# Kernel tuning notes

Hardware: AMD Instinct MI355X
Metric: run time of the kernel (lower is better)

## Reference

```python
import jax, jax.numpy as jnp
import numpy as np

VOCAB, HIDDEN, EMBED = 30522, 768, 512
PAD_INDEX = 0
NEG_SLOPE = 0.1


def setup_inputs() -> dict:
    key = jax.random.key(0)
    k1, k2, k3, k4 = jax.random.split(key, 4)
    words = jax.random.randint(k1, (16, 512, 4), 0, VOCAB, dtype=jnp.int64) if jax.config.jax_enable_x64 else jax.random.randint(k1, (16, 512, 4), 0, VOCAB, dtype=jnp.int32)
    embed_table = jax.random.normal(k2, (VOCAB, HIDDEN), dtype=jnp.float32) * 0.02
    w_ffn = jax.random.normal(k3, (HIDDEN, EMBED), dtype=jnp.float32) * 0.02
    b_ffn = jax.random.normal(k4, (EMBED,), dtype=jnp.float32) * 0.02
    return {"words": words, "embed_table": embed_table, "w_ffn": w_ffn, "b_ffn": b_ffn}


def reference(words, embed_table, w_ffn, b_ffn):
    # words: [B, S, W] subword ids; pad_index marks padding subwords/words.
    B, S, W = words.shape
    sub_mask = words != PAD_INDEX                      # [B,S,W] valid subwords
    word_valid = jnp.any(sub_mask, axis=-1)            # [B,S]  words with >=1 subword
    lens = jnp.sum(word_valid, axis=-1)                # [B]    valid words per sequence

    # Stub of transformer last_hidden_state: per-token hidden vectors. [B,S,W,H]
    x = embed_table[words]

    # Masked mean over subwords of each word (segment mean-pool).
    m = sub_mask[..., None].astype(x.dtype)
    cnt = jnp.maximum(jnp.sum(sub_mask, axis=-1), 1)[..., None].astype(x.dtype)
    pooled = jnp.sum(x * m, axis=2) / cnt              # [B,S,H]

    # pad = x[0, -1] of flattened [B, S*W, H] == hidden of last flat token of batch 0
    pad_vec = x[0, -1, -1]                             # [H]

    # Stable compaction: valid words first (mirrors pop-in-order + pad append).
    order = jnp.argsort(jnp.logical_not(word_valid), axis=1, stable=True)  # [B,S]
    pooled_c = jnp.take_along_axis(pooled, order[..., None], axis=1)       # [B,S,H]
    keep = (jnp.arange(S)[None, :] < lens[:, None])[..., None]             # [B,S,1]
    x_seq = jnp.where(keep, pooled_c, pad_vec)         # [B,S,H]

    # FFN: Linear + LeakyReLU(0.1)
    return jax.nn.leaky_relu(x_seq @ w_ffn + b_ffn, NEG_SLOPE)
```

## Files before the change

kernel.cpp:

```cpp
#include <hip/hip_runtime.h>
#include <stdint.h>

#define HIDDEN 768
#define EMBED  512
#define BATCH  16
#define SEQ    512
#define NWORDS (BATCH*SEQ)
#define PAD_FLAT_IDX 2047
#define NEG_SLOPE 0.1f

__device__ __forceinline__ unsigned short f2bf(float f) {
    unsigned int x = __float_as_uint(f);
    unsigned int r = x + 0x7fffu + ((x >> 16) & 1u);
    return (unsigned short)(r >> 16);
}

__global__ __launch_bounds__(256) void prep_kernel(const int* __restrict__ words,
                                                   const float* __restrict__ w,
                                                   int* __restrict__ dest,
                                                   unsigned short* __restrict__ wt) {
    if (blockIdx.x < BATCH) {
        int b = blockIdx.x;
        int t = threadIdx.x;
        int s0 = 2 * t, s1 = 2 * t + 1;
        int4 wa = ((const int4*)words)[b * SEQ + s0];
        int4 wb = ((const int4*)words)[b * SEQ + s1];
        bool v0 = (wa.x | wa.y | wa.z | wa.w) != 0;
        bool v1 = (wb.x | wb.y | wb.z | wb.w) != 0;

        unsigned long long m0 = __ballot(v0);
        unsigned long long m1 = __ballot(v1);
        int lane = t & 63;
        int wave = t >> 6;
        unsigned long long below = (1ull << lane) - 1ull;
        int pre = __popcll(m0 & below) + __popcll(m1 & below);
        __shared__ int wsum[4];
        if (lane == 0) wsum[wave] = __popcll(m0) + __popcll(m1);
        __syncthreads();
        int off = 0, tot = 0;
#pragma unroll
        for (int i = 0; i < 4; ++i) {
            int x = wsum[i];
            if (i < wave) off += x;
            tot += x;
        }
        int vp0 = off + pre;
        int vp1 = vp0 + (v0 ? 1 : 0);
        int d0 = v0 ? vp0 : (tot + (s0 - vp0));
        int d1 = v1 ? vp1 : (tot + (s1 - vp1));
        dest[b * SEQ + s0] = b * SEQ + d0;
        dest[b * SEQ + s1] = b * SEQ + d1;
    } else {
        __shared__ float tile[32][33];
        int bid = blockIdx.x - BATCH;
        int k0 = (bid % (HIDDEN / 32)) * 32;
        int n0 = (bid / (HIDDEN / 32)) * 32;
        int tc = threadIdx.x & 31;
        int tr = threadIdx.x >> 5;
#pragma unroll
        for (int i = 0; i < 4; ++i) {
            int r = tr + i * 8;
            tile[r][tc] = w[(size_t)(k0 + r) * EMBED + n0 + tc];
        }
        __syncthreads();
#pragma unroll
        for (int i = 0; i < 4; ++i) {
            int r = tr + i * 8;
            wt[(size_t)(n0 + r) * HIDDEN + k0 + tc] = f2bf(tile[tc][r]);
        }
    }
}

__global__ __launch_bounds__(192) void pool_kernel(const int* __restrict__ words,
                                                   const float* __restrict__ table,
                                                   const int* __restrict__ dest,
                                                   unsigned short* __restrict__ xseq) {
    int word = blockIdx.x;
    int t = threadIdx.x;
    int drow = dest[word];
    int4 w4 = ((const int4*)words)[word];
    int cnt = (w4.x != 0) + (w4.y != 0) + (w4.z != 0) + (w4.w != 0);

    float ax = 0.f, ay = 0.f, az = 0.f, aw = 0.f;
    if (cnt == 0) {
        int pid = words[PAD_FLAT_IDX];
        float4 v = ((const float4*)(table + (size_t)pid * HIDDEN))[t];
        ax = v.x; ay = v.y; az = v.z; aw = v.w;
    } else {
        if (w4.x != 0) { float4 v = ((const float4*)(table + (size_t)w4.x * HIDDEN))[t]; ax += v.x; ay += v.y; az += v.z; aw += v.w; }
        if (w4.y != 0) { float4 v = ((const float4*)(table + (size_t)w4.y * HIDDEN))[t]; ax += v.x; ay += v.y; az += v.z; aw += v.w; }
        if (w4.z != 0) { float4 v = ((const float4*)(table + (size_t)w4.z * HIDDEN))[t]; ax += v.x; ay += v.y; az += v.z; aw += v.w; }
        if (w4.w != 0) { float4 v = ((const float4*)(table + (size_t)w4.w * HIDDEN))[t]; ax += v.x; ay += v.y; az += v.z; aw += v.w; }
        float inv = 1.0f / (float)cnt;
        ax *= inv; ay *= inv; az *= inv; aw *= inv;
    }
    ushort4 o;
    o.x = f2bf(ax); o.y = f2bf(ay); o.z = f2bf(az); o.w = f2bf(aw);
    ((ushort4*)(xseq + (size_t)drow * HIDDEN))[t] = o;
}

typedef __attribute__((ext_vector_type(8))) short bf16x8;
typedef __attribute__((ext_vector_type(4))) float f32x4;

__device__ __forceinline__ void load_lds16(const void* g, void* l) {
    __builtin_amdgcn_global_load_lds(
        (const __attribute__((address_space(1))) unsigned int*)g,
        (__attribute__((address_space(3))) unsigned int*)l,
        16, 0, 0);
}

#define BM 128
#define BN 64
#define BK 32

__global__ __launch_bounds__(256) void gemm_kernel(const unsigned short* __restrict__ A,
                                                   const unsigned short* __restrict__ Bt,
                                                   const float* __restrict__ bias,
                                                   float* __restrict__ out) {
    __shared__ unsigned short sA[BM * BK];
    __shared__ unsigned short sB[BN * BK];

    int tid  = threadIdx.x;
    int m0   = blockIdx.x * BM;
    int n0   = blockIdx.y * BN;
    int wave = tid >> 6;
    int lane = tid & 63;
    int wr   = wave >> 1;
    int wc   = wave & 1;
    int quad = lane >> 4;
    int l16  = lane & 15;

    f32x4 acc[4][2] = {};

    const unsigned short* ga0 = A  + (size_t)(m0 + (tid >> 2)) * HIDDEN + (tid & 3) * 8;
    const unsigned short* ga1 = A  + (size_t)(m0 + 64 + (tid >> 2)) * HIDDEN + (tid & 3) * 8;
    const unsigned short* gb  = Bt + (size_t)(n0 + (tid >> 2)) * HIDDEN + (tid & 3) * 8;

    for (int k0 = 0; k0 < HIDDEN; k0 += BK) {
        load_lds16(ga0 + k0, &sA[tid * 8]);
        load_lds16(ga1 + k0, &sA[(256 + tid) * 8]);
        load_lds16(gb  + k0, &sB[tid * 8]);
        __syncthreads();

        bf16x8 af[4], bf[2];
#pragma unroll
        for (int mt = 0; mt < 4; ++mt)
            af[mt] = *(const bf16x8*)&sA[(wr * 64 + mt * 16 + l16) * BK + quad * 8];
#pragma unroll
        for (int nt = 0; nt < 2; ++nt)
            bf[nt] = *(const bf16x8*)&sB[(wc * 32 + nt * 16 + l16) * BK + quad * 8];

#pragma unroll
        for (int mt = 0; mt < 4; ++mt)
#pragma unroll
            for (int nt = 0; nt < 2; ++nt)
                acc[mt][nt] = __builtin_amdgcn_mfma_f32_16x16x32_bf16(
                    af[mt], bf[nt], acc[mt][nt], 0, 0, 0);
        __syncthreads();
    }

#pragma unroll
    for (int nt = 0; nt < 2; ++nt) {
        int col = n0 + wc * 32 + nt * 16 + l16;
        float bv = bias[col];
#pragma unroll
        for (int mt = 0; mt < 4; ++mt) {
            int rbase = m0 + wr * 64 + mt * 16 + quad * 4;
#pragma unroll
            for (int r = 0; r < 4; ++r) {
                float v = acc[mt][nt][r] + bv;
                v = (v > 0.f) ? v : v * NEG_SLOPE;
                out[(size_t)(rbase + r) * EMBED + col] = v;
            }
        }
    }
}

extern "C" void kernel_launch(void* const* d_in, const int* in_sizes, int n_in,
                              void* d_out, int out_size, void* d_ws, size_t ws_size,
                              hipStream_t stream) {
    (void)in_sizes; (void)n_in; (void)out_size; (void)ws_size;
    const int*   words = (const int*)d_in[0];
    const float* table = (const float*)d_in[1];
    const float* wffn  = (const float*)d_in[2];
    const float* bffn  = (const float*)d_in[3];
    float* out = (float*)d_out;

    char* ws = (char*)d_ws;
    unsigned short* xseq = (unsigned short*)ws;
    unsigned short* wt   = (unsigned short*)(ws + 12582912);
    int*            dest = (int*)(ws + 12582912 + 786432);

    prep_kernel<<<BATCH + (HIDDEN / 32) * (EMBED / 32), 256, 0, stream>>>(words, wffn, dest, wt);
    pool_kernel<<<NWORDS, 192, 0, stream>>>(words, table, dest, xseq);
    gemm_kernel<<<dim3(NWORDS / BM, EMBED / BN), 256, 0, stream>>>(xseq, wt, bffn, out);
}
```

Measured before the change: 162.5 us.

## Fuse subword mean-pooling into GEMM with compacted id lists

After: 174.2 us. +7.2%, slower.

```diff
diff --git a/kernel.cpp b/kernel.cpp
--- a/kernel.cpp
+++ b/kernel.cpp
@@ -8,6 +8,8 @@
 #define NWORDS (BATCH*SEQ)
 #define PAD_FLAT_IDX 2047
 #define NEG_SLOPE 0.1f
+#define SA_LD 776
+#define BM 32
 
 __device__ __forceinline__ unsigned short f2bf(float f) {
     unsigned int x = __float_as_uint(f);
@@ -17,7 +19,8 @@
 
 __global__ __launch_bounds__(256) void prep_kernel(const int* __restrict__ words,
                                                    const float* __restrict__ w,
-                                                   int* __restrict__ dest,
+                                                   int4* __restrict__ ids4,
+                                                   int* __restrict__ cnts,
                                                    unsigned short* __restrict__ wt) {
     if (blockIdx.x < BATCH) {
         int b = blockIdx.x;
@@ -48,8 +51,29 @@
         int vp1 = vp0 + (v0 ? 1 : 0);
         int d0 = v0 ? vp0 : (tot + (s0 - vp0));
         int d1 = v1 ? vp1 : (tot + (s1 - vp1));
-        dest[b * SEQ + s0] = b * SEQ + d0;
-        dest[b * SEQ + s1] = b * SEQ + d1;
+
+        int pid = words[PAD_FLAT_IDX];
+
+        {
+            int id[4] = {wa.x, wa.y, wa.z, wa.w};
+            int o[4] = {0, 0, 0, 0};
+            int c = 0;
+#pragma unroll
+            for (int j = 0; j < 4; ++j) if (id[j] != 0) o[c++] = id[j];
+            if (c == 0) { o[0] = pid; c = 1; }
+            ids4[b * SEQ + d0] = make_int4(o[0], o[1], o[2], o[3]);
+            cnts[b * SEQ + d0] = c;
+        }
+        {
+            int id[4] = {wb.x, wb.y, wb.z, wb.w};
+            int o[4] = {0, 0, 0, 0};
+            int c = 0;
+#pragma unroll
+            for (int j = 0; j < 4; ++j) if (id[j] != 0) o[c++] = id[j];
+            if (c == 0) { o[0] = pid; c = 1; }
+            ids4[b * SEQ + d1] = make_int4(o[0], o[1], o[2], o[3]);
+            cnts[b * SEQ + d1] = c;
+        }
     } else {
         __shared__ float tile[32][33];
         int bid = blockIdx.x - BATCH;
@@ -71,34 +95,6 @@
     }
 }
 
-__global__ __launch_bounds__(192) void pool_kernel(const int* __restrict__ words,
-                                                   const float* __restrict__ table,
-                                                   const int* __restrict__ dest,
-                                                   unsigned short* __restrict__ xseq) {
-    int word = blockIdx.x;
-    int t = threadIdx.x;
-    int drow = dest[word];
-    int4 w4 = ((const int4*)words)[word];
-    int cnt = (w4.x != 0) + (w4.y != 0) + (w4.z != 0) + (w4.w != 0);
-
-    float ax = 0.f, ay = 0.f, az = 0.f, aw = 0.f;
-    if (cnt == 0) {
-        int pid = words[PAD_FLAT_IDX];
-        float4 v = ((const float4*)(table + (size_t)pid * HIDDEN))[t];
-        ax = v.x; ay = v.y; az = v.z; aw = v.w;
-    } else {
-        if (w4.x != 0) { float4 v = ((const float4*)(table + (size_t)w4.x * HIDDEN))[t]; ax += v.x; ay += v.y; az += v.z; aw += v.w; }
-        if (w4.y != 0) { float4 v = ((const float4*)(table + (size_t)w4.y * HIDDEN))[t]; ax += v.x; ay += v.y; az += v.z; aw += v.w; }
-        if (w4.z != 0) { float4 v = ((const float4*)(table + (size_t)w4.z * HIDDEN))[t]; ax += v.x; ay += v.y; az += v.z; aw += v.w; }
-        if (w4.w != 0) { float4 v = ((const float4*)(table + (size_t)w4.w * HIDDEN))[t]; ax += v.x; ay += v.y; az += v.z; aw += v.w; }
-        float inv = 1.0f / (float)cnt;
-        ax *= inv; ay *= inv; az *= inv; aw *= inv;
-    }
-    ushort4 o;
-    o.x = f2bf(ax); o.y = f2bf(ay); o.z = f2bf(az); o.w = f2bf(aw);
-    ((ushort4*)(xseq + (size_t)drow * HIDDEN))[t] = o;
-}
-
 typedef __attribute__((ext_vector_type(8))) short bf16x8;
 typedef __attribute__((ext_vector_type(4))) float f32x4;
 
@@ -109,63 +105,86 @@
         16, 0, 0);
 }
 
-#define BM 128
-#define BN 64
-#define BK 32
-
-__global__ __launch_bounds__(256) void gemm_kernel(const unsigned short* __restrict__ A,
-                                                   const unsigned short* __restrict__ Bt,
-                                                   const float* __restrict__ bias,
-                                                   float* __restrict__ out) {
-    __shared__ unsigned short sA[BM * BK];
-    __shared__ unsigned short sB[BN * BK];
+__global__ __launch_bounds__(256) void fused_kernel(const int4* __restrict__ ids4,
+                                                    const int* __restrict__ cnts,
+                                                    const float* __restrict__ table,
+                                                    const unsigned short* __restrict__ Bt,
+                                                    const float* __restrict__ bias,
+                                                    float* __restrict__ out) {
+    __shared__ unsigned short sA[BM * SA_LD];
+    __shared__ unsigned short sB[512 * 32];
 
     int tid  = threadIdx.x;
-    int m0   = blockIdx.x * BM;
-    int n0   = blockIdx.y * BN;
     int wave = tid >> 6;
     int lane = tid & 63;
-    int wr   = wave >> 1;
-    int wc   = wave & 1;
+    int m0   = blockIdx.x * BM;
+
+#pragma unroll 2
+    for (int i = 0; i < 8; ++i) {
+        int rl  = i * 4 + wave;
+        int row = m0 + rl;
+        int4 w4 = ids4[row];
+        int cnt = cnts[row];
+        int id[4] = {w4.x, w4.y, w4.z, w4.w};
+        float sx[3] = {0.f, 0.f, 0.f}, sy[3] = {0.f, 0.f, 0.f};
+        float sz[3] = {0.f, 0.f, 0.f}, sw[3] = {0.f, 0.f, 0.f};
+#pragma unroll
+        for (int j = 0; j < 4; ++j) {
+            if (j < cnt) {
+                const float4* rp = (const float4*)(table + (size_t)id[j] * HIDDEN);
+#pragma unroll
+                for (int c = 0; c < 3; ++c) {
+                    float4 v = rp[lane + 64 * c];
+                    sx[c] += v.x; sy[c] += v.y; sz[c] += v.z; sw[c] += v.w;
+                }
+            }
+        }
+        float inv = 1.0f / (float)cnt;
+#pragma unroll
+        for (int c = 0; c < 3; ++c) {
+            ushort4 o;
+            o.x = f2bf(sx[c] * inv); o.y = f2bf(sy[c] * inv);
+            o.z = f2bf(sz[c] * inv); o.w = f2bf(sw[c] * inv);
+            *(ushort4*)&sA[rl * SA_LD + (lane + 64 * c) * 4] = o;
+        }
+    }
+
     int quad = lane >> 4;
     int l16  = lane & 15;
-
-    f32x4 acc[4][2] = {};
-
-    const unsigned short* ga0 = A  + (size_t)(m0 + (tid >> 2)) * HIDDEN + (tid & 3) * 8;
-    const unsigned short* ga1 = A  + (size_t)(m0 + 64 + (tid >> 2)) * HIDDEN + (tid & 3) * 8;
-    const unsigned short* gb  = Bt + (size_t)(n0 + (tid >> 2)) * HIDDEN + (tid & 3) * 8;
-
-    for (int k0 = 0; k0 < HIDDEN; k0 += BK) {
-        load_lds16(ga0 + k0, &sA[tid * 8]);
-        load_lds16(ga1 + k0, &sA[(256 + tid) * 8]);
-        load_lds16(gb  + k0, &sB[tid * 8]);
-        __syncthreads();
-
-        bf16x8 af[4], bf[2];
-#pragma unroll
-        for (int mt = 0; mt < 4; ++mt)
-            af[mt] = *(const bf16x8*)&sA[(wr * 64 + mt * 16 + l16) * BK + quad * 8];
-#pragma unroll
-        for (int nt = 0; nt < 2; ++nt)
-            bf[nt] = *(const bf16x8*)&sB[(wc * 32 + nt * 16 + l16) * BK + quad * 8];
-
-#pragma unroll
-        for (int mt = 0; mt < 4; ++mt)
-#pragma unroll
-            for (int nt = 0; nt < 2; ++nt)
+    f32x4 acc[2][8] = {};
+
+    const unsigned short* gb = Bt + (size_t)(tid >> 2) * HIDDEN + (tid & 3) * 8;
+
+    for (int k0 = 0; k0 < HIDDEN; k0 += 32) {
+#pragma unroll
+        for (int j = 0; j < 8; ++j)
+            load_lds16(gb + (size_t)j * 64 * HIDDEN + k0, &sB[(tid + 256 * j) * 8]);
+        __syncthreads();
+
+        bf16x8 af[2], bfr[8];
+#pragma unroll
+        for (int mt = 0; mt < 2; ++mt)
+            af[mt] = *(const bf16x8*)&sA[(mt * 16 + l16) * SA_LD + k0 + quad * 8];
+#pragma unroll
+        for (int nt = 0; nt < 8; ++nt)
+            bfr[nt] = *(const bf16x8*)&sB[(wave * 128 + nt * 16 + l16) * 32 + quad * 8];
+
+#pragma unroll
+        for (int mt = 0; mt < 2; ++mt)
+#pragma unroll
+            for (int nt = 0; nt < 8; ++nt)
                 acc[mt][nt] = __builtin_amdgcn_mfma_f32_16x16x32_bf16(
-                    af[mt], bf[nt], acc[mt][nt], 0, 0, 0);
-        __syncthreads();
-    }
-
-#pragma unroll
-    for (int nt = 0; nt < 2; ++nt) {
-        int col = n0 + wc * 32 + nt * 16 + l16;
+                    af[mt], bfr[nt], acc[mt][nt], 0, 0, 0);
+        __syncthreads();
+    }
+
+#pragma unroll
+    for (int nt = 0; nt < 8; ++nt) {
+        int col = wave * 128 + nt * 16 + l16;
         float bv = bias[col];
 #pragma unroll
-        for (int mt = 0; mt < 4; ++mt) {
-            int rbase = m0 + wr * 64 + mt * 16 + quad * 4;
+        for (int mt = 0; mt < 2; ++mt) {
+            int rbase = m0 + mt * 16 + quad * 4;
 #pragma unroll
             for (int r = 0; r < 4; ++r) {
                 float v = acc[mt][nt][r] + bv;
@@ -187,11 +206,11 @@
     float* out = (float*)d_out;
 
     char* ws = (char*)d_ws;
-    unsigned short* xseq = (unsigned short*)ws;
-    unsigned short* wt   = (unsigned short*)(ws + 12582912);
-    int*            dest = (int*)(ws + 12582912 + 786432);
-
-    prep_kernel<<<BATCH + (HIDDEN / 32) * (EMBED / 32), 256, 0, stream>>>(words, wffn, dest, wt);
-    pool_kernel<<<NWORDS, 192, 0, stream>>>(words, table, dest, xseq);
-    gemm_kernel<<<dim3(NWORDS / BM, EMBED / BN), 256, 0, stream>>>(xseq, wt, bffn, out);
-}
+    unsigned short* wt   = (unsigned short*)ws;
+    int4*           ids4 = (int4*)(ws + 786432);
+    int*            cnts = (int*)(ws + 786432 + 131072);
+
+    prep_kernel<<<BATCH + (HIDDEN / 32) * (EMBED / 32), 256, 0, stream>>>(
+        words, wffn, ids4, cnts, wt);
+    fused_kernel<<<NWORDS / BM, 256, 0, stream>>>(ids4, cnts, table, wt, bffn, out);
+}
```

## Load GEMM fragments directly from global memory, dropping LDS staging

Applied to the files above, without the earlier changes.

After: 183.6 us. 13.0% more time.

```diff
diff --git a/kernel.cpp b/kernel.cpp
--- a/kernel.cpp
+++ b/kernel.cpp
@@ -102,70 +102,51 @@
 typedef __attribute__((ext_vector_type(8))) short bf16x8;
 typedef __attribute__((ext_vector_type(4))) float f32x4;
 
-__device__ __forceinline__ void load_lds16(const void* g, void* l) {
-    __builtin_amdgcn_global_load_lds(
-        (const __attribute__((address_space(1))) unsigned int*)g,
-        (__attribute__((address_space(3))) unsigned int*)l,
-        16, 0, 0);
-}
-
 #define BM 128
 #define BN 64
-#define BK 32
 
 __global__ __launch_bounds__(256) void gemm_kernel(const unsigned short* __restrict__ A,
                                                    const unsigned short* __restrict__ Bt,
                                                    const float* __restrict__ bias,
                                                    float* __restrict__ out) {
-    __shared__ unsigned short sA[BM * BK];
-    __shared__ unsigned short sB[BN * BK];
-
     int tid  = threadIdx.x;
-    int m0   = blockIdx.x * BM;
-    int n0   = blockIdx.y * BN;
     int wave = tid >> 6;
     int lane = tid & 63;
-    int wr   = wave >> 1;
-    int wc   = wave & 1;
     int quad = lane >> 4;
     int l16  = lane & 15;
+    int m0   = blockIdx.x * BM + wave * 32;
+    int n0   = blockIdx.y * BN;
 
-    f32x4 acc[4][2] = {};
+    f32x4 acc[2][4] = {};
 
-    const unsigned short* ga0 = A  + (size_t)(m0 + (tid >> 2)) * HIDDEN + (tid & 3) * 8;
-    const unsigned short* ga1 = A  + (size_t)(m0 + 64 + (tid >> 2)) * HIDDEN + (tid & 3) * 8;
-    const unsigned short* gb  = Bt + (size_t)(n0 + (tid >> 2)) * HIDDEN + (tid & 3) * 8;
+    const unsigned short* pa = A  + (size_t)(m0 + l16) * HIDDEN + quad * 8;
+    const unsigned short* pb = Bt + (size_t)(n0 + l16) * HIDDEN + quad * 8;
 
-    for (int k0 = 0; k0 < HIDDEN; k0 += BK) {
-        load_lds16(ga0 + k0, &sA[tid * 8]);
-        load_lds16(ga1 + k0, &sA[(256 + tid) * 8]);
-        load_lds16(gb  + k0, &sB[tid * 8]);
-        __syncthreads();
-
-        bf16x8 af[4], bf[2];
+#pragma unroll 2
+    for (int k0 = 0; k0 < HIDDEN; k0 += 32) {
+        bf16x8 af[2], bfr[4];
 #pragma unroll
-        for (int mt = 0; mt < 4; ++mt)
-            af[mt] = *(const bf16x8*)&sA[(wr * 64 + mt * 16 + l16) * BK + quad * 8];
+        for (int mt = 0; mt < 2; ++mt)
+            af[mt] = *(const bf16x8*)(pa + (size_t)mt * 16 * HIDDEN + k0);
 #pragma unroll
-        for (int nt = 0; nt < 2; ++nt)
-            bf[nt] = *(const bf16x8*)&sB[(wc * 32 + nt * 16 + l16) * BK + quad * 8];
+        for (int nt = 0; nt < 4; ++nt)
+            bfr[nt] = *(const bf16x8*)(pb + (size_t)nt * 16 * HIDDEN + k0);
 
 #pragma unroll
-        for (int mt = 0; mt < 4; ++mt)
+        for (int mt = 0; mt < 2; ++mt)
 #pragma unroll
-            for (int nt = 0; nt < 2; ++nt)
+            for (int nt = 0; nt < 4; ++nt)
                 acc[mt][nt] = __builtin_amdgcn_mfma_f32_16x16x32_bf16(
-                    af[mt], bf[nt], acc[mt][nt], 0, 0, 0);
-        __syncthreads();
+                    af[mt], bfr[nt], acc[mt][nt], 0, 0, 0);
     }
 
 #pragma unroll
-    for (int nt = 0; nt < 2; ++nt) {
-        int col = n0 + wc * 32 + nt * 16 + l16;
+    for (int nt = 0; nt < 4; ++nt) {
+        int col = n0 + nt * 16 + l16;
         float bv = bias[col];
 #pragma unroll
-        for (int mt = 0; mt < 4; ++mt) {
-            int rbase = m0 + wr * 64 + mt * 16 + quad * 4;
+        for (int mt = 0; mt < 2; ++mt) {
+            int rbase = m0 + mt * 16 + quad * 4;
 #pragma unroll
             for (int r = 0; r < 4; ++r) {
                 float v = acc[mt][nt][r] + bv;
```

## Fuse compaction, pooling and weight transpose into one kernel launch

Applied to the files above, without the earlier changes.

Measured after the change: 160.8 us. About the same (-1.0%).

```diff
diff --git a/kernel.cpp b/kernel.cpp
--- a/kernel.cpp
+++ b/kernel.cpp
@@ -8,6 +8,7 @@
 #define NWORDS (BATCH*SEQ)
 #define PAD_FLAT_IDX 2047
 #define NEG_SLOPE 0.1f
+#define NPOOLBLK 2048
 
 __device__ __forceinline__ unsigned short f2bf(float f) {
     unsigned int x = __float_as_uint(f);
@@ -15,44 +16,82 @@
     return (unsigned short)(r >> 16);
 }
 
-__global__ __launch_bounds__(256) void prep_kernel(const int* __restrict__ words,
-                                                   const float* __restrict__ w,
-                                                   int* __restrict__ dest,
-                                                   unsigned short* __restrict__ wt) {
-    if (blockIdx.x < BATCH) {
-        int b = blockIdx.x;
-        int t = threadIdx.x;
-        int s0 = 2 * t, s1 = 2 * t + 1;
-        int4 wa = ((const int4*)words)[b * SEQ + s0];
-        int4 wb = ((const int4*)words)[b * SEQ + s1];
-        bool v0 = (wa.x | wa.y | wa.z | wa.w) != 0;
-        bool v1 = (wb.x | wb.y | wb.z | wb.w) != 0;
-
-        unsigned long long m0 = __ballot(v0);
-        unsigned long long m1 = __ballot(v1);
-        int lane = t & 63;
-        int wave = t >> 6;
-        unsigned long long below = (1ull << lane) - 1ull;
-        int pre = __popcll(m0 & below) + __popcll(m1 & below);
-        __shared__ int wsum[4];
-        if (lane == 0) wsum[wave] = __popcll(m0) + __popcll(m1);
-        __syncthreads();
-        int off = 0, tot = 0;
-#pragma unroll
-        for (int i = 0; i < 4; ++i) {
-            int x = wsum[i];
-            if (i < wave) off += x;
-            tot += x;
-        }
-        int vp0 = off + pre;
-        int vp1 = vp0 + (v0 ? 1 : 0);
-        int d0 = v0 ? vp0 : (tot + (s0 - vp0));
-        int d1 = v1 ? vp1 : (tot + (s1 - vp1));
-        dest[b * SEQ + s0] = b * SEQ + d0;
-        dest[b * SEQ + s1] = b * SEQ + d1;
+__global__ __launch_bounds__(256) void combo_kernel(const int* __restrict__ words,
+                                                    const float* __restrict__ w,
+                                                    const float* __restrict__ table,
+                                                    unsigned short* __restrict__ xseq,
+                                                    unsigned short* __restrict__ wt) {
+    if (blockIdx.x < NPOOLBLK) {
+        __shared__ unsigned long long mask[8];
+        int b    = blockIdx.x >> 7;
+        int wave = threadIdx.x >> 6;
+        int lane = threadIdx.x & 63;
+
+        int p0 = wave * 64 + lane;
+        int p1 = p0 + 256;
+        int4 wa = ((const int4*)words)[b * SEQ + p0];
+        int4 wb = ((const int4*)words)[b * SEQ + p1];
+        unsigned long long mlo = __ballot((wa.x | wa.y | wa.z | wa.w) != 0);
+        unsigned long long mhi = __ballot((wb.x | wb.y | wb.z | wb.w) != 0);
+        if (lane == 0) { mask[wave] = mlo; mask[4 + wave] = mhi; }
+        __syncthreads();
+
+        int s = (blockIdx.x & 127) * 4 + wave;
+        int seg = s >> 6;
+        int bit = s & 63;
+        int vp = 0, tot = 0;
+#pragma unroll
+        for (int i = 0; i < 8; ++i) {
+            unsigned long long m = mask[i];
+            int c = __popcll(m);
+            if (i < seg) vp += c;
+            tot += c;
+        }
+        unsigned long long mseg = mask[seg];
+        vp += __popcll(mseg & ((1ull << bit) - 1ull));
+        bool valid = (mseg >> bit) & 1ull;
+        int d = valid ? vp : (tot + (s - vp));
+        int drow = b * SEQ + d;
+
+        int4 w4 = ((const int4*)words)[b * SEQ + s];
+        int cnt = (w4.x != 0) + (w4.y != 0) + (w4.z != 0) + (w4.w != 0);
+
+        float sx[3] = {0.f, 0.f, 0.f}, sy[3] = {0.f, 0.f, 0.f};
+        float sz[3] = {0.f, 0.f, 0.f}, sw[3] = {0.f, 0.f, 0.f};
+        if (cnt == 0) {
+            int pid = words[PAD_FLAT_IDX];
+            const float4* rp = (const float4*)(table + (size_t)pid * HIDDEN);
+#pragma unroll
+            for (int c = 0; c < 3; ++c) {
+                float4 v = rp[lane + 64 * c];
+                sx[c] = v.x; sy[c] = v.y; sz[c] = v.z; sw[c] = v.w;
+            }
+            cnt = 1;
+        } else {
+            int id[4] = {w4.x, w4.y, w4.z, w4.w};
+#pragma unroll
+            for (int j = 0; j < 4; ++j) {
+                if (id[j] != 0) {
+                    const float4* rp = (const float4*)(table + (size_t)id[j] * HIDDEN);
+#pragma unroll
+                    for (int c = 0; c < 3; ++c) {
+                        float4 v = rp[lane + 64 * c];
+                        sx[c] += v.x; sy[c] += v.y; sz[c] += v.z; sw[c] += v.w;
+                    }
+                }
+            }
+        }
+        float inv = 1.0f / (float)cnt;
+#pragma unroll
+        for (int c = 0; c < 3; ++c) {
+            ushort4 o;
+            o.x = f2bf(sx[c] * inv); o.y = f2bf(sy[c] * inv);
+            o.z = f2bf(sz[c] * inv); o.w = f2bf(sw[c] * inv);
+            *(ushort4*)&xseq[(size_t)drow * HIDDEN + (lane + 64 * c) * 4] = o;
+        }
     } else {
         __shared__ float tile[32][33];
-        int bid = blockIdx.x - BATCH;
+        int bid = blockIdx.x - NPOOLBLK;
         int k0 = (bid % (HIDDEN / 32)) * 32;
         int n0 = (bid / (HIDDEN / 32)) * 32;
         int tc = threadIdx.x & 31;
@@ -69,34 +108,6 @@
             wt[(size_t)(n0 + r) * HIDDEN + k0 + tc] = f2bf(tile[tc][r]);
         }
     }
-}
-
-__global__ __launch_bounds__(192) void pool_kernel(const int* __restrict__ words,
-                                                   const float* __restrict__ table,
-                                                   const int* __restrict__ dest,
-                                                   unsigned short* __restrict__ xseq) {
-    int word = blockIdx.x;
-    int t = threadIdx.x;
-    int drow = dest[word];
-    int4 w4 = ((const int4*)words)[word];
-    int cnt = (w4.x != 0) + (w4.y != 0) + (w4.z != 0) + (w4.w != 0);
-
-    float ax = 0.f, ay = 0.f, az = 0.f, aw = 0.f;
-    if (cnt == 0) {
-        int pid = words[PAD_FLAT_IDX];
-        float4 v = ((const float4*)(table + (size_t)pid * HIDDEN))[t];
-        ax = v.x; ay = v.y; az = v.z; aw = v.w;
-    } else {
-        if (w4.x != 0) { float4 v = ((const float4*)(table + (size_t)w4.x * HIDDEN))[t]; ax += v.x; ay += v.y; az += v.z; aw += v.w; }
-        if (w4.y != 0) { float4 v = ((const float4*)(table + (size_t)w4.y * HIDDEN))[t]; ax += v.x; ay += v.y; az += v.z; aw += v.w; }
-        if (w4.z != 0) { float4 v = ((const float4*)(table + (size_t)w4.z * HIDDEN))[t]; ax += v.x; ay += v.y; az += v.z; aw += v.w; }
-        if (w4.w != 0) { float4 v = ((const float4*)(table + (size_t)w4.w * HIDDEN))[t]; ax += v.x; ay += v.y; az += v.z; aw += v.w; }
-        float inv = 1.0f / (float)cnt;
-        ax *= inv; ay *= inv; az *= inv; aw *= inv;
-    }
-    ushort4 o;
-    o.x = f2bf(ax); o.y = f2bf(ay); o.z = f2bf(az); o.w = f2bf(aw);
-    ((ushort4*)(xseq + (size_t)drow * HIDDEN))[t] = o;
 }
 
 typedef __attribute__((ext_vector_type(8))) short bf16x8;
@@ -142,20 +153,20 @@
         load_lds16(gb  + k0, &sB[tid * 8]);
         __syncthreads();
 
-        bf16x8 af[4], bf[2];
+        bf16x8 af[4], bfr[2];
 #pragma unroll
         for (int mt = 0; mt < 4; ++mt)
             af[mt] = *(const bf16x8*)&sA[(wr * 64 + mt * 16 + l16) * BK + quad * 8];
 #pragma unroll
         for (int nt = 0; nt < 2; ++nt)
-            bf[nt] = *(const bf16x8*)&sB[(wc * 32 + nt * 16 + l16) * BK + quad * 8];
+            bfr[nt] = *(const bf16x8*)&sB[(wc * 32 + nt * 16 + l16) * BK + quad * 8];
 
 #pragma unroll
         for (int mt = 0; mt < 4; ++mt)
 #pragma unroll
             for (int nt = 0; nt < 2; ++nt)
                 acc[mt][nt] = __builtin_amdgcn_mfma_f32_16x16x32_bf16(
-                    af[mt], bf[nt], acc[mt][nt], 0, 0, 0);
+                    af[mt], bfr[nt], acc[mt][nt], 0, 0, 0);
         __syncthreads();
     }
 
@@ -189,9 +200,8 @@
     char* ws = (char*)d_ws;
     unsigned short* xseq = (unsigned short*)ws;
     unsigned short* wt   = (unsigned short*)(ws + 12582912);
-    int*            dest = (int*)(ws + 12582912 + 786432);
-
-    prep_kernel<<<BATCH + (HIDDEN / 32) * (EMBED / 32), 256, 0, stream>>>(words, wffn, dest, wt);
-    pool_kernel<<<NWORDS, 192, 0, stream>>>(words, table, dest, xseq);
+
+    combo_kernel<<<NPOOLBLK + (HIDDEN / 32) * (EMBED / 32), 256, 0, stream>>>(
+        words, wffn, table, xseq, wt);
     gemm_kernel<<<dim3(NWORDS / BM, EMBED / BN), 256, 0, stream>>>(xseq, wt, bffn, out);
 }
```
